# Kernel tuning notes

Measured on AMD Instinct MI355X. Metric: run time of the kernel, lower is better.

## Reference

```python
import jax, jax.numpy as jnp
import numpy as np

B, N, F, E = 2048, 64, 32, 5
U1, U2, UA = 128, 64, 128

def setup_inputs() -> dict:
    key = jax.random.key(0)
    ks = jax.random.split(key, 16)
    inp = {
        'adjacency': jax.random.uniform(ks[0], (B, N, N, E), dtype=jnp.float32),
        'hidden': jnp.zeros((B, 1), dtype=jnp.float32),
        'node': jax.random.normal(ks[1], (B, N, F), dtype=jnp.float32),
        # conv layer 1: per-edge-type dense F->U1 (stacked), plus node dense F->U1
        'W1': jax.random.normal(ks[2], (E - 1, F, U1), dtype=jnp.float32) * 0.05,
        'b1': jnp.zeros((E - 1, U1), dtype=jnp.float32),
        'V1': jax.random.normal(ks[3], (F, U1), dtype=jnp.float32) * 0.05,
        'c1': jnp.zeros((U1,), dtype=jnp.float32),
        # conv layer 2: annotations (U1+F)->U2, node F->U2
        'W2': jax.random.normal(ks[4], (E - 1, U1 + F, U2), dtype=jnp.float32) * 0.05,
        'b2': jnp.zeros((E - 1, U2), dtype=jnp.float32),
        'V2': jax.random.normal(ks[5], (F, U2), dtype=jnp.float32) * 0.05,
        'c2': jnp.zeros((U2,), dtype=jnp.float32),
        # aggregation: (U2+F)->UA gates
        'Wi': jax.random.normal(ks[6], (U2 + F, UA), dtype=jnp.float32) * 0.05,
        'bi': jnp.zeros((UA,), dtype=jnp.float32),
        'Wj': jax.random.normal(ks[7], (U2 + F, UA), dtype=jnp.float32) * 0.05,
        'bj': jnp.zeros((UA,), dtype=jnp.float32),
    }
    return inp


def _gconv(adj_t, annotations, node, W, b, V, c):
    # adj_t: [B,E-1,N,N]; annotations: [B,N,Fa]; node: [B,N,F]
    h = jnp.einsum('bnf,efu->benu', annotations, W) + b[None, :, None, :]
    h = jnp.einsum('bemn,benu->bemu', adj_t, h)          # adjacency-weighted sum
    out = h.sum(axis=1) + node @ V + c                   # [B,N,U]
    return jnp.tanh(out)


def reference(adjacency, hidden, node, W1, b1, V1, c1, W2, b2, V2, c2, Wi, bi, Wj, bj):
    # drop edge type 0, transpose to [B,E-1,N,N]
    adj_t = jnp.transpose(adjacency[:, :, :, 1:], (0, 3, 1, 2))
    # hidden is rank-2 at entry -> first layer uses node only
    h1 = _gconv(adj_t, node, node, W1, b1, V1, c1)                       # [B,N,U1]
    h2 = _gconv(adj_t, jnp.concatenate((h1, node), -1), node, W2, b2, V2, c2)  # [B,N,U2]
    # encoder-level annotations: (output, node) since hidden is rank-2
    ann = jnp.concatenate((h2, node), -1)                                # [B,N,U2+F]
    i = jax.nn.sigmoid(ann @ Wi + bi)
    j = jnp.tanh(ann @ Wj + bj)
    out = jnp.tanh(jnp.sum(i * j, axis=1))                               # [B,UA]
    return out
```

## Files before the change

kernel.cpp:

```cpp
#include <hip/hip_runtime.h>

typedef _Float16 f16;
typedef f16  f16x8 __attribute__((ext_vector_type(8)));
typedef f16  f16x4 __attribute__((ext_vector_type(4)));
typedef float f32x4 __attribute__((ext_vector_type(4)));
typedef unsigned int u32;

#define W1T_HI 0
#define W1T_LO 16384
#define V1T_HI 32768
#define V1T_LO 36864
#define W2T_HI 40960
#define W2T_LO 81920
#define V2T_HI 122880
#define V2T_LO 124928
#define WIT_HI 126976
#define WIT_LO 139264
#define WJT_HI 151552
#define WJT_LO 163840
#define WS_SRC 88064

#define ADJB_HI 0
#define ADJB_LO 32768
#define ANNB_HI 49152
#define ANNB_LO 65536
#define PTB     73728
#define LDS_BYTES 81920

__device__ __forceinline__ f32x4 mfma16(f16x8 a, f16x8 b, f32x4 c){
  return __builtin_amdgcn_mfma_f32_16x16x32_f16(a, b, c, 0, 0, 0);
}
__device__ __forceinline__ float fast_tanh(float x){
  float e = __expf(2.f * x);
  return 1.f - 2.f * __builtin_amdgcn_rcpf(e + 1.f);
}
__device__ __forceinline__ float fast_sigmoid(float x){
  return __builtin_amdgcn_rcpf(1.f + __expf(-x));
}

__device__ __forceinline__ unsigned char enc1(float lo){
  f16 h = (f16)lo;
  unsigned short u = __builtin_bit_cast(unsigned short, h);
  return (unsigned char)(((u32)u + 0x80u) >> 8);
}
__device__ __forceinline__ void enc8(unsigned char* p, const float* lo){
  u32 a = 0, b = 0;
  #pragma unroll
  for (int j = 0; j < 4; ++j) a |= (u32)enc1(lo[j]) << (8*j);
  #pragma unroll
  for (int j = 0; j < 4; ++j) b |= (u32)enc1(lo[4+j]) << (8*j);
  uint2 v = {a, b};
  *(uint2*)p = v;
}
__device__ __forceinline__ u32 enc4(const float* lo){
  return (u32)enc1(lo[0]) | ((u32)enc1(lo[1]) << 8)
       | ((u32)enc1(lo[2]) << 16) | ((u32)enc1(lo[3]) << 24);
}
__device__ __forceinline__ f16x8 dec8(const unsigned char* p){
  uint2 d = *(const uint2*)p;
  u32 w[4];
  w[0] = __builtin_amdgcn_perm(0u, d.x, 0x010c000cu);
  w[1] = __builtin_amdgcn_perm(0u, d.x, 0x030c020cu);
  w[2] = __builtin_amdgcn_perm(0u, d.y, 0x010c000cu);
  w[3] = __builtin_amdgcn_perm(0u, d.y, 0x030c020cu);
  f16x8 r; __builtin_memcpy(&r, w, 16);
  return r;
}

__global__ void prep_weights(const float* __restrict__ W1, const float* __restrict__ V1,
                             const float* __restrict__ W2, const float* __restrict__ V2,
                             const float* __restrict__ Wi, const float* __restrict__ Wj,
                             f16* __restrict__ ws){
  int i = blockIdx.x * 256 + threadIdx.x;
  if (i >= WS_SRC) return;
  float v; int hi_off, lo_off, idx;
  int j = i;
  if (j < 16384){ int e = j >> 12, u = (j >> 5) & 127, f = j & 31;
    v = W1[(e*32 + f)*128 + u]; hi_off = W1T_HI; lo_off = W1T_LO; idx = j; }
  else if ((j -= 16384) < 4096){ int u = j >> 5, f = j & 31;
    v = V1[f*128 + u]; hi_off = V1T_HI; lo_off = V1T_LO; idx = j; }
  else if ((j -= 4096) < 40960){ int e = j / 10240, r = j % 10240, u = r / 160, k = r % 160;
    v = W2[e*10240 + k*64 + u]; hi_off = W2T_HI; lo_off = W2T_LO; idx = j; }
  else if ((j -= 40960) < 2048){ int u = j >> 5, f = j & 31;
    v = V2[f*64 + u]; hi_off = V2T_HI; lo_off = V2T_LO; idx = j; }
  else if ((j -= 2048) < 12288){ int ua = j / 96, k = j % 96;
    v = Wi[k*128 + ua]; hi_off = WIT_HI; lo_off = WIT_LO; idx = j; }
  else { j -= 12288; int ua = j / 96, k = j % 96;
    v = Wj[k*128 + ua]; hi_off = WJT_HI; lo_off = WJT_LO; idx = j; }
  f16 h = (f16)v;
  ws[hi_off + idx] = h;
  ws[lo_off + idx] = (f16)(v - (float)h);
}

__global__ __launch_bounds__(512, 4) void encoder_main(
    const float* __restrict__ adj, const float* __restrict__ node,
    const float* __restrict__ b1, const float* __restrict__ c1,
    const float* __restrict__ b2, const float* __restrict__ c2,
    const float* __restrict__ bi, const float* __restrict__ bj,
    const f16* __restrict__ wb, float* __restrict__ out)
{
  extern __shared__ unsigned char ldsb[];
  f16* adjh            = (f16*)(ldsb + ADJB_HI);
  unsigned char* adjl  = ldsb + ADJB_LO;
  f16* annh            = (f16*)(ldsb + ANNB_HI);
  unsigned char* annl  = ldsb + ANNB_LO;
  float* scr           = (float*)(ldsb + ANNB_HI);
  f16* nodeH           = (f16*)(ldsb + PTB);
  f16* nodeLo          = (f16*)(ldsb + PTB + 4096);

  const int tid  = threadIdx.x;
  const int w    = tid >> 6;
  const int lane = tid & 63;
  const int q    = lane >> 4;
  const int l15  = lane & 15;
  const int eg   = w >> 2;
  const int w4   = w & 3;
  const int b    = blockIdx.x;
  const f32x4 z4 = {0.f, 0.f, 0.f, 0.f};

  unsigned char* ptb = ldsb + ((w < 4) ? (PTB + w*2048) : (ANNB_HI + (w - 4)*2048));
  unsigned char* ptl = ldsb + ANNB_LO + w*1024;
  const int ptrow  = l15 * 128;
  const int ptlrow = l15 * 64;

  {
    const float* ap = adj + (size_t)b * 20480;
    #pragma unroll
    for (int i = 0; i < 4; ++i){
      int fu = tid + 512*i;
      int e = fu >> 9, m = (fu >> 3) & 63, uc = fu & 7;
      const float* p = ap + (m*64 + uc*8)*5 + e + 1;
      float v[8], lo[8]; f16x8 hi;
      #pragma unroll
      for (int jj = 0; jj < 8; ++jj) v[jj] = p[jj*5];
      #pragma unroll
      for (int jj = 0; jj < 8; ++jj){
        f16 h = (f16)v[jj]; hi[jj] = h; lo[jj] = v[jj] - (float)h;
      }
      int off = e*4096 + m*64 + ((uc ^ (m & 7)) * 8);
      *(f16x8*)&adjh[off] = hi;
      enc8(&adjl[off], lo);
    }
    if (tid < 256){
      const float* np = node + (size_t)b * 2048 + (tid & 63)*32 + (tid >> 6)*8;
      float4 a = *(const float4*)np, c = *(const float4*)(np + 4);
      float v[8] = {a.x, a.y, a.z, a.w, c.x, c.y, c.z, c.w};
      f16x8 hi, lo;
      #pragma unroll
      for (int jj = 0; jj < 8; ++jj){
        f16 h = (f16)v[jj]; hi[jj] = h; lo[jj] = (f16)(v[jj] - (float)h);
      }
      int n = tid & 63, un = tid >> 6;
      *(f16x8*)&nodeH [n*32 + ((un ^ (n & 3)) * 8)] = hi;
      *(f16x8*)&nodeLo[n*32 + ((un ^ (n & 3)) * 8)] = lo;
    }
  }
  __syncthreads();

  f16x8 anh[4], anl[4];
  #pragma unroll
  for (int mt = 0; mt < 4; ++mt){
    anh[mt] = *(const f16x8*)&nodeH [(mt*16 + l15)*32 + ((q ^ (l15 & 3)) * 8)];
    anl[mt] = *(const f16x8*)&nodeLo[(mt*16 + l15)*32 + ((q ^ (l15 & 3)) * 8)];
  }
  __syncthreads();

  f32x4 acc1[4][2];
  #pragma unroll
  for (int mt = 0; mt < 4; ++mt){ acc1[mt][0] = z4; acc1[mt][1] = z4; }

  #pragma unroll
  for (int i = 0; i < 2; ++i){
    const int e = eg*2 + i;
    #pragma unroll
    for (int ut = 0; ut < 2; ++ut){
      const int u = w4*32 + ut*16 + l15;
      f16x8 wh = *(const f16x8*)&wb[W1T_HI + (e*128 + u)*32 + q*8];
      f16x8 wl = *(const f16x8*)&wb[W1T_LO + (e*128 + u)*32 + q*8];
      float bias = b1[e*128 + u];
      #pragma unroll
      for (int mt = 0; mt < 4; ++mt){
        f32x4 pf = mfma16(anh[mt], wh, z4);
        pf = mfma16(anl[mt], wh, pf);
        pf = mfma16(anh[mt], wl, pf);
        f16x4 ph; float lo4[4];
        #pragma unroll
        for (int r = 0; r < 4; ++r){
          float v = pf[r] + bias;
          f16 h = (f16)v; ph[r] = h; lo4[r] = v - (float)h;
        }
        int unit = ((mt*2 + (q >> 1)) ^ (l15 & 7));
        *(f16x4*)(ptb + ptrow + unit*16 + (q & 1)*8) = ph;
        *(u32*)(ptl + ptlrow + unit*8 + (q & 1)*4) = enc4(lo4);
      }
      #pragma unroll
      for (int ks = 0; ks < 2; ++ks){
        int pu = ((ks*4 + q) ^ (l15 & 7));
        f16x8 bph = *(const f16x8*)(ptb + ptrow + pu*16);
        f16x8 bpl = dec8(ptl + ptlrow + pu*8);
        #pragma unroll
        for (int mt = 0; mt < 4; ++mt){
          int off = e*4096 + (mt*16 + l15)*64 + (((ks*4 + q) ^ (l15 & 7)) * 8);
          f16x8 ah = *(const f16x8*)&adjh[off];
          f16x8 al = dec8(&adjl[off]);
          acc1[mt][ut] = mfma16(ah, bph, acc1[mt][ut]);
          acc1[mt][ut] = mfma16(al, bph, acc1[mt][ut]);
          acc1[mt][ut] = mfma16(ah, bpl, acc1[mt][ut]);
        }
      }
    }
  }
  __syncthreads();

  if (eg == 0){
    #pragma unroll
    for (int ut = 0; ut < 2; ++ut){
      const int u = w4*32 + ut*16 + l15;
      f16x8 wh = *(const f16x8*)&wb[V1T_HI + u*32 + q*8];
      f16x8 wl = *(const f16x8*)&wb[V1T_LO + u*32 + q*8];
      #pragma unroll
      for (int mt = 0; mt < 4; ++mt){
        acc1[mt][ut] = mfma16(anh[mt], wh, acc1[mt][ut]);
        acc1[mt][ut] = mfma16(anl[mt], wh, acc1[mt][ut]);
        acc1[mt][ut] = mfma16(anh[mt], wl, acc1[mt][ut]);
      }
    }
  } else {
    #pragma unroll
    for (int mt = 0; mt < 4; ++mt)
      #pragma unroll
      for (int ut = 0; ut < 2; ++ut)
        #pragma unroll
        for (int r = 0; r < 4; ++r){
          int n = mt*16 + q*4 + r;
          int u = w4*32 + ut*16 + l15;
          scr[n*128 + (u ^ ((n & 4) << 2))] = acc1[mt][ut][r];
        }
  }
  __syncthreads();
  if (eg == 0){
    #pragma unroll
    for (int mt = 0; mt < 4; ++mt)
      #pragma unroll
      for (int ut = 0; ut < 2; ++ut)
        #pragma unroll
        for (int r = 0; r < 4; ++r){
          int n = mt*16 + q*4 + r;
          int u = w4*32 + ut*16 + l15;
          acc1[mt][ut][r] += scr[n*128 + (u ^ ((n & 4) << 2))];
        }
  }
  __syncthreads();
  if (eg == 0){
    #pragma unroll
    for (int ut = 0; ut < 2; ++ut){
      const int u = w4*32 + ut*16 + l15;
      float cv = c1[u];
      #pragma unroll
      for (int mt = 0; mt < 4; ++mt)
        #pragma unroll
        for (int r = 0; r < 4; ++r){
          float h = fast_tanh(acc1[mt][ut][r] + cv);
          f16 hh = (f16)h;
          int row = mt*16 + q*4 + r;
          int unit = ((u >> 3) ^ (row & 7));
          annh[row*128 + unit*8 + (u & 7)] = hh;
          annl[row*128 + unit*8 + (u & 7)] = enc1(h - (float)hh);
        }
    }
  }
  __syncthreads();

  const int u2 = w4*16 + l15;
  f32x4 qf[2][4];
  #pragma unroll
  for (int mt = 0; mt < 4; ++mt){
    #pragma unroll
    for (int i = 0; i < 2; ++i){
      const int e = eg*2 + i;
      const f16* w2h = &wb[W2T_HI + (e*64 + u2)*160];
      const f16* w2l = &wb[W2T_LO + (e*64 + u2)*160];
      f16x8 wnh = *(const f16x8*)&w2h[4*32 + q*8];
      f16x8 wnl = *(const f16x8*)&w2l[4*32 + q*8];
      f32x4 t = mfma16(anh[mt], wnh, z4);
      t = mfma16(anl[mt], wnh, t);
      t = mfma16(anh[mt], wnl, t);
      #pragma unroll
      for (int ks = 0; ks < 4; ++ks){
        int off = (mt*16 + l15)*128 + (((ks*4 + q) ^ (l15 & 7)) * 8);
        f16x8 axh = *(const f16x8*)&annh[off];
        f16x8 axl = dec8(&annl[off]);
        f16x8 wh = *(const f16x8*)&w2h[ks*32 + q*8];
        f16x8 wl = *(const f16x8*)&w2l[ks*32 + q*8];
        t = mfma16(axh, wh, t);
        t = mfma16(axl, wh, t);
        t = mfma16(axh, wl, t);
      }
      qf[i][mt] = t;
    }
  }
  __syncthreads();

  f32x4 acc2[4];
  #pragma unroll
  for (int mt = 0; mt < 4; ++mt) acc2[mt] = z4;
  #pragma unroll
  for (int i = 0; i < 2; ++i){
    const int e = eg*2 + i;
    float bias = b2[e*64 + u2];
    #pragma unroll
    for (int mt = 0; mt < 4; ++mt){
      f16x4 ph; float lo4[4];
      #pragma unroll
      for (int r = 0; r < 4; ++r){
        float v = qf[i][mt][r] + bias;
        f16 h = (f16)v; ph[r] = h; lo4[r] = v - (float)h;
      }
      int unit = ((mt*2 + (q >> 1)) ^ (l15 & 7));
      *(f16x4*)(ptb + ptrow + unit*16 + (q & 1)*8) = ph;
      *(u32*)(ptl + ptlrow + unit*8 + (q & 1)*4) = enc4(lo4);
    }
    #pragma unroll
    for (int ks = 0; ks < 2; ++ks){
      int pu = ((ks*4 + q) ^ (l15 & 7));
      f16x8 bph = *(const f16x8*)(ptb + ptrow + pu*16);
      f16x8 bpl = dec8(ptl + ptlrow + pu*8);
      #pragma unroll
      for (int mt = 0; mt < 4; ++mt){
        int off = e*4096 + (mt*16 + l15)*64 + (((ks*4 + q) ^ (l15 & 7)) * 8);
        f16x8 ah = *(const f16x8*)&adjh[off];
        f16x8 al = dec8(&adjl[off]);
        acc2[mt] = mfma16(ah, bph, acc2[mt]);
        acc2[mt] = mfma16(al, bph, acc2[mt]);
        acc2[mt] = mfma16(ah, bpl, acc2[mt]);
      }
    }
  }
  __syncthreads();
  if (eg == 0){
    f16x8 wh = *(const f16x8*)&wb[V2T_HI + u2*32 + q*8];
    f16x8 wl = *(const f16x8*)&wb[V2T_LO + u2*32 + q*8];
    #pragma unroll
    for (int mt = 0; mt < 4; ++mt){
      acc2[mt] = mfma16(anh[mt], wh, acc2[mt]);
      acc2[mt] = mfma16(anl[mt], wh, acc2[mt]);
      acc2[mt] = mfma16(anh[mt], wl, acc2[mt]);
    }
  } else {
    #pragma unroll
    for (int mt = 0; mt < 4; ++mt)
      #pragma unroll
      for (int r = 0; r < 4; ++r){
        int n = mt*16 + q*4 + r;
        scr[n*64 + (u2 ^ ((n & 4) << 2))] = acc2[mt][r];
      }
  }
  __syncthreads();
  if (eg == 0){
    #pragma unroll
    for (int mt = 0; mt < 4; ++mt)
      #pragma unroll
      for (int r = 0; r < 4; ++r){
        int n = mt*16 + q*4 + r;
        acc2[mt][r] += scr[n*64 + (u2 ^ ((n & 4) << 2))];
      }
  }
  __syncthreads();
  if (eg == 0){
    float cv = c2[u2];
    const int uc = 64 + u2;
    #pragma unroll
    for (int mt = 0; mt < 4; ++mt)
      #pragma unroll
      for (int r = 0; r < 4; ++r){
        float h = fast_tanh(acc2[mt][r] + cv);
        f16 hh = (f16)h;
        int row = mt*16 + q*4 + r;
        int unit = ((uc >> 3) ^ (row & 7));
        annh[row*128 + unit*8 + (uc & 7)] = hh;
        annl[row*128 + unit*8 + (uc & 7)] = enc1(h - (float)hh);
      }
  }
  __syncthreads();

  const int ua = w*16 + l15;
  float bib = bi[ua], bjb = bj[ua];
  f32x4 iacc[4], jacc[4];
  #pragma unroll
  for (int mt = 0; mt < 4; ++mt){ iacc[mt] = z4; jacc[mt] = z4; }
  #pragma unroll
  for (int ks = 0; ks < 3; ++ks){
    f16x8 wih = *(const f16x8*)&wb[WIT_HI + ua*96 + ks*32 + q*8];
    f16x8 wil = *(const f16x8*)&wb[WIT_LO + ua*96 + ks*32 + q*8];
    f16x8 wjh = *(const f16x8*)&wb[WJT_HI + ua*96 + ks*32 + q*8];
    f16x8 wjl = *(const f16x8*)&wb[WJT_LO + ua*96 + ks*32 + q*8];
    if (ks < 2){
      #pragma unroll
      for (int mt = 0; mt < 4; ++mt){
        int off = (mt*16 + l15)*128 + (((8 + ks*4 + q) ^ (l15 & 7)) * 8);
        f16x8 gh = *(const f16x8*)&annh[off];
        f16x8 gl = dec8(&annl[off]);
        iacc[mt] = mfma16(gh, wih, iacc[mt]);
        iacc[mt] = mfma16(gl, wih, iacc[mt]);
        iacc[mt] = mfma16(gh, wil, iacc[mt]);
        jacc[mt] = mfma16(gh, wjh, jacc[mt]);
        jacc[mt] = mfma16(gl, wjh, jacc[mt]);
        jacc[mt] = mfma16(gh, wjl, jacc[mt]);
      }
    } else {
      #pragma unroll
      for (int mt = 0; mt < 4; ++mt){
        iacc[mt] = mfma16(anh[mt], wih, iacc[mt]);
        iacc[mt] = mfma16(anl[mt], wih, iacc[mt]);
        iacc[mt] = mfma16(anh[mt], wil, iacc[mt]);
        jacc[mt] = mfma16(anh[mt], wjh, jacc[mt]);
        jacc[mt] = mfma16(anl[mt], wjh, jacc[mt]);
        jacc[mt] = mfma16(anh[mt], wjl, jacc[mt]);
      }
    }
  }
  float s = 0.f;
  #pragma unroll
  for (int mt = 0; mt < 4; ++mt)
    #pragma unroll
    for (int r = 0; r < 4; ++r)
      s += fast_sigmoid(iacc[mt][r] + bib) * fast_tanh(jacc[mt][r] + bjb);
  s += __shfl_xor(s, 16);
  s += __shfl_xor(s, 32);
  if (q == 0) out[(size_t)b*128 + ua] = fast_tanh(s);
}

extern "C" void kernel_launch(void* const* d_in, const int* in_sizes, int n_in,
                              void* d_out, int out_size, void* d_ws, size_t ws_size,
                              hipStream_t stream) {
  (void)in_sizes; (void)n_in; (void)out_size; (void)ws_size;
  const float* adj  = (const float*)d_in[0];
  const float* node = (const float*)d_in[2];
  const float* W1   = (const float*)d_in[3];
  const float* b1   = (const float*)d_in[4];
  const float* V1   = (const float*)d_in[5];
  const float* c1   = (const float*)d_in[6];
  const float* W2   = (const float*)d_in[7];
  const float* b2   = (const float*)d_in[8];
  const float* V2   = (const float*)d_in[9];
  const float* c2   = (const float*)d_in[10];
  const float* Wi   = (const float*)d_in[11];
  const float* bi   = (const float*)d_in[12];
  const float* Wj   = (const float*)d_in[13];
  const float* bj   = (const float*)d_in[14];
  f16* wb    = (f16*)d_ws;
  float* out = (float*)d_out;

  hipFuncSetAttribute((const void*)encoder_main,
                      hipFuncAttributeMaxDynamicSharedMemorySize, LDS_BYTES);

  prep_weights<<<(WS_SRC + 255) / 256, 256, 0, stream>>>(W1, V1, W2, V2, Wi, Wj, wb);
  encoder_main<<<2048, 512, LDS_BYTES, stream>>>(adj, node, b1, c1, b2, c2, bi, bj, wb, out);
}
```

Before: 388.4 us.

## Reload node tiles from LDS on demand and shrink layer-1 reduction scratch

Removes the long-lived register copies of the node fragments (anh/anl). The node hi/lo tiles are kept in LDS and reloaded with volatile loads at each use, and the adjacency fragments are also read with volatile loads to stop the compiler hoisting them. All per-wave P-tile scratch now lives in the ANN region, and the cross-eg layer-1 reduction is split into two half-width passes so the scratch is 64 columns wide. The layer-2 node/annotation GEMM loop is reordered so both edge types share each weight load. The goal is lower VGPR pressure, which may allow higher occupancy, at the cost of extra LDS traffic and two more barriers.

```diff
diff --git a/kernel.cpp b/kernel.cpp
--- a/kernel.cpp
+++ b/kernel.cpp
@@ -5,6 +5,7 @@
 typedef f16  f16x4 __attribute__((ext_vector_type(4)));
 typedef float f32x4 __attribute__((ext_vector_type(4)));
 typedef unsigned int u32;
+typedef unsigned long long u64;
 
 #define W1T_HI 0
 #define W1T_LO 16384
@@ -56,13 +57,27 @@
   return (u32)enc1(lo[0]) | ((u32)enc1(lo[1]) << 8)
        | ((u32)enc1(lo[2]) << 16) | ((u32)enc1(lo[3]) << 24);
 }
+__device__ __forceinline__ f16x8 dec8_w(u32 dx, u32 dy){
+  u32 w[4];
+  w[0] = __builtin_amdgcn_perm(0u, dx, 0x010c000cu);
+  w[1] = __builtin_amdgcn_perm(0u, dx, 0x030c020cu);
+  w[2] = __builtin_amdgcn_perm(0u, dy, 0x010c000cu);
+  w[3] = __builtin_amdgcn_perm(0u, dy, 0x030c020cu);
+  f16x8 r; __builtin_memcpy(&r, w, 16);
+  return r;
+}
 __device__ __forceinline__ f16x8 dec8(const unsigned char* p){
   uint2 d = *(const uint2*)p;
-  u32 w[4];
-  w[0] = __builtin_amdgcn_perm(0u, d.x, 0x010c000cu);
-  w[1] = __builtin_amdgcn_perm(0u, d.x, 0x030c020cu);
-  w[2] = __builtin_amdgcn_perm(0u, d.y, 0x010c000cu);
-  w[3] = __builtin_amdgcn_perm(0u, d.y, 0x030c020cu);
+  return dec8_w(d.x, d.y);
+}
+__device__ __forceinline__ f16x8 dec8v(const unsigned char* p){
+  u64 v = *(const volatile u64*)p;
+  return dec8_w((u32)v, (u32)(v >> 32));
+}
+__device__ __forceinline__ f16x8 lds16v(const f16* p){
+  u64 a = ((const volatile u64*)p)[0];
+  u64 b = ((const volatile u64*)p)[1];
+  u64 w[2] = {a, b};
   f16x8 r; __builtin_memcpy(&r, w, 16);
   return r;
 }
@@ -118,10 +133,15 @@
   const int b    = blockIdx.x;
   const f32x4 z4 = {0.f, 0.f, 0.f, 0.f};
 
-  unsigned char* ptb = ldsb + ((w < 4) ? (PTB + w*2048) : (ANNB_HI + (w - 4)*2048));
+  unsigned char* ptb = ldsb + ANNB_HI + w*2048;
   unsigned char* ptl = ldsb + ANNB_LO + w*1024;
   const int ptrow  = l15 * 128;
   const int ptlrow = l15 * 64;
+
+  #define LOAD_NODE(mt, nh, nl) {                                   \
+    int no_ = ((mt)*16 + l15)*32 + ((q ^ (l15 & 3)) * 8);           \
+    nh = lds16v(&nodeH[no_]);                                       \
+    nl = lds16v(&nodeLo[no_]); }
 
   {
     const float* ap = adj + (size_t)b * 20480;
@@ -157,14 +177,6 @@
   }
   __syncthreads();
 
-  f16x8 anh[4], anl[4];
-  #pragma unroll
-  for (int mt = 0; mt < 4; ++mt){
-    anh[mt] = *(const f16x8*)&nodeH [(mt*16 + l15)*32 + ((q ^ (l15 & 3)) * 8)];
-    anl[mt] = *(const f16x8*)&nodeLo[(mt*16 + l15)*32 + ((q ^ (l15 & 3)) * 8)];
-  }
-  __syncthreads();
-
   f32x4 acc1[4][2];
   #pragma unroll
   for (int mt = 0; mt < 4; ++mt){ acc1[mt][0] = z4; acc1[mt][1] = z4; }
@@ -180,9 +192,10 @@
       float bias = b1[e*128 + u];
       #pragma unroll
       for (int mt = 0; mt < 4; ++mt){
-        f32x4 pf = mfma16(anh[mt], wh, z4);
-        pf = mfma16(anl[mt], wh, pf);
-        pf = mfma16(anh[mt], wl, pf);
+        f16x8 nh, nl; LOAD_NODE(mt, nh, nl);
+        f32x4 pf = mfma16(nh, wh, z4);
+        pf = mfma16(nl, wh, pf);
+        pf = mfma16(nh, wl, pf);
         f16x4 ph; float lo4[4];
         #pragma unroll
         for (int r = 0; r < 4; ++r){
@@ -201,8 +214,8 @@
         #pragma unroll
         for (int mt = 0; mt < 4; ++mt){
           int off = e*4096 + (mt*16 + l15)*64 + (((ks*4 + q) ^ (l15 & 7)) * 8);
-          f16x8 ah = *(const f16x8*)&adjh[off];
-          f16x8 al = dec8(&adjl[off]);
+          f16x8 ah = lds16v(&adjh[off]);
+          f16x8 al = dec8v(&adjl[off]);
           acc1[mt][ut] = mfma16(ah, bph, acc1[mt][ut]);
           acc1[mt][ut] = mfma16(al, bph, acc1[mt][ut]);
           acc1[mt][ut] = mfma16(ah, bpl, acc1[mt][ut]);
@@ -220,12 +233,13 @@
       f16x8 wl = *(const f16x8*)&wb[V1T_LO + u*32 + q*8];
       #pragma unroll
       for (int mt = 0; mt < 4; ++mt){
-        acc1[mt][ut] = mfma16(anh[mt], wh, acc1[mt][ut]);
-        acc1[mt][ut] = mfma16(anl[mt], wh, acc1[mt][ut]);
-        acc1[mt][ut] = mfma16(anh[mt], wl, acc1[mt][ut]);
-      }
-    }
-  } else {
+        f16x8 nh, nl; LOAD_NODE(mt, nh, nl);
+        acc1[mt][ut] = mfma16(nh, wh, acc1[mt][ut]);
+        acc1[mt][ut] = mfma16(nl, wh, acc1[mt][ut]);
+        acc1[mt][ut] = mfma16(nh, wl, acc1[mt][ut]);
+      }
+    }
+  } else if (w4 < 2){
     #pragma unroll
     for (int mt = 0; mt < 4; ++mt)
       #pragma unroll
@@ -233,12 +247,12 @@
         #pragma unroll
         for (int r = 0; r < 4; ++r){
           int n = mt*16 + q*4 + r;
-          int u = w4*32 + ut*16 + l15;
-          scr[n*128 + (u ^ ((n & 4) << 2))] = acc1[mt][ut][r];
-        }
-  }
-  __syncthreads();
-  if (eg == 0){
+          int ul = w4*32 + ut*16 + l15;
+          scr[n*64 + (ul ^ ((n & 4) << 2))] = acc1[mt][ut][r];
+        }
+  }
+  __syncthreads();
+  if (eg == 0 && w4 < 2){
     #pragma unroll
     for (int mt = 0; mt < 4; ++mt)
       #pragma unroll
@@ -246,8 +260,34 @@
         #pragma unroll
         for (int r = 0; r < 4; ++r){
           int n = mt*16 + q*4 + r;
-          int u = w4*32 + ut*16 + l15;
-          acc1[mt][ut][r] += scr[n*128 + (u ^ ((n & 4) << 2))];
+          int ul = w4*32 + ut*16 + l15;
+          acc1[mt][ut][r] += scr[n*64 + (ul ^ ((n & 4) << 2))];
+        }
+  }
+  __syncthreads();
+  if (eg == 1 && w4 >= 2){
+    #pragma unroll
+    for (int mt = 0; mt < 4; ++mt)
+      #pragma unroll
+      for (int ut = 0; ut < 2; ++ut)
+        #pragma unroll
+        for (int r = 0; r < 4; ++r){
+          int n = mt*16 + q*4 + r;
+          int ul = (w4 - 2)*32 + ut*16 + l15;
+          scr[n*64 + (ul ^ ((n & 4) << 2))] = acc1[mt][ut][r];
+        }
+  }
+  __syncthreads();
+  if (eg == 0 && w4 >= 2){
+    #pragma unroll
+    for (int mt = 0; mt < 4; ++mt)
+      #pragma unroll
+      for (int ut = 0; ut < 2; ++ut)
+        #pragma unroll
+        for (int r = 0; r < 4; ++r){
+          int n = mt*16 + q*4 + r;
+          int ul = (w4 - 2)*32 + ut*16 + l15;
+          acc1[mt][ut][r] += scr[n*64 + (ul ^ ((n & 4) << 2))];
         }
   }
   __syncthreads();
@@ -272,31 +312,46 @@
   __syncthreads();
 
   const int u2 = w4*16 + l15;
+  const int e0 = eg*2, e1 = eg*2 + 1;
+  const f16* w2h0 = &wb[W2T_HI + (e0*64 + u2)*160];
+  const f16* w2l0 = &wb[W2T_LO + (e0*64 + u2)*160];
+  const f16* w2h1 = &wb[W2T_HI + (e1*64 + u2)*160];
+  const f16* w2l1 = &wb[W2T_LO + (e1*64 + u2)*160];
   f32x4 qf[2][4];
-  #pragma unroll
-  for (int mt = 0; mt < 4; ++mt){
-    #pragma unroll
-    for (int i = 0; i < 2; ++i){
-      const int e = eg*2 + i;
-      const f16* w2h = &wb[W2T_HI + (e*64 + u2)*160];
-      const f16* w2l = &wb[W2T_LO + (e*64 + u2)*160];
-      f16x8 wnh = *(const f16x8*)&w2h[4*32 + q*8];
-      f16x8 wnl = *(const f16x8*)&w2l[4*32 + q*8];
-      f32x4 t = mfma16(anh[mt], wnh, z4);
-      t = mfma16(anl[mt], wnh, t);
-      t = mfma16(anh[mt], wnl, t);
-      #pragma unroll
-      for (int ks = 0; ks < 4; ++ks){
-        int off = (mt*16 + l15)*128 + (((ks*4 + q) ^ (l15 & 7)) * 8);
-        f16x8 axh = *(const f16x8*)&annh[off];
-        f16x8 axl = dec8(&annl[off]);
-        f16x8 wh = *(const f16x8*)&w2h[ks*32 + q*8];
-        f16x8 wl = *(const f16x8*)&w2l[ks*32 + q*8];
-        t = mfma16(axh, wh, t);
-        t = mfma16(axl, wh, t);
-        t = mfma16(axh, wl, t);
-      }
-      qf[i][mt] = t;
+  {
+    f16x8 wA = *(const f16x8*)&w2h0[128 + q*8];
+    f16x8 wB = *(const f16x8*)&w2l0[128 + q*8];
+    f16x8 wC = *(const f16x8*)&w2h1[128 + q*8];
+    f16x8 wD = *(const f16x8*)&w2l1[128 + q*8];
+    #pragma unroll
+    for (int mt = 0; mt < 4; ++mt){
+      f16x8 nh, nl; LOAD_NODE(mt, nh, nl);
+      f32x4 t0 = mfma16(nh, wA, z4);
+      t0 = mfma16(nl, wA, t0);
+      t0 = mfma16(nh, wB, t0);
+      f32x4 t1 = mfma16(nh, wC, z4);
+      t1 = mfma16(nl, wC, t1);
+      t1 = mfma16(nh, wD, t1);
+      qf[0][mt] = t0; qf[1][mt] = t1;
+    }
+  }
+  #pragma unroll
+  for (int ks = 0; ks < 4; ++ks){
+    f16x8 wA = *(const f16x8*)&w2h0[ks*32 + q*8];
+    f16x8 wB = *(const f16x8*)&w2l0[ks*32 + q*8];
+    f16x8 wC = *(const f16x8*)&w2h1[ks*32 + q*8];
+    f16x8 wD = *(const f16x8*)&w2l1[ks*32 + q*8];
+    #pragma unroll
+    for (int mt = 0; mt < 4; ++mt){
+      int off = (mt*16 + l15)*128 + (((ks*4 + q) ^ (l15 & 7)) * 8);
+      f16x8 axh = *(const f16x8*)&annh[off];
+      f16x8 axl = dec8(&annl[off]);
+      qf[0][mt] = mfma16(axh, wA, qf[0][mt]);
+      qf[0][mt] = mfma16(axl, wA, qf[0][mt]);
+      qf[0][mt] = mfma16(axh, wB, qf[0][mt]);
+      qf[1][mt] = mfma16(axh, wC, qf[1][mt]);
+      qf[1][mt] = mfma16(axl, wC, qf[1][mt]);
+      qf[1][mt] = mfma16(axh, wD, qf[1][mt]);
     }
   }
   __syncthreads();
@@ -342,9 +397,10 @@
     f16x8 wl = *(const f16x8*)&wb[V2T_LO + u2*32 + q*8];
     #pragma unroll
     for (int mt = 0; mt < 4; ++mt){
-      acc2[mt] = mfma16(anh[mt], wh, acc2[mt]);
-      acc2[mt] = mfma16(anl[mt], wh, acc2[mt]);
-      acc2[mt] = mfma16(anh[mt], wl, acc2[mt]);
+      f16x8 nh, nl; LOAD_NODE(mt, nh, nl);
+      acc2[mt] = mfma16(nh, wh, acc2[mt]);
+      acc2[mt] = mfma16(nl, wh, acc2[mt]);
+      acc2[mt] = mfma16(nh, wl, acc2[mt]);
     }
   } else {
     #pragma unroll
@@ -410,12 +466,13 @@
     } else {
       #pragma unroll
       for (int mt = 0; mt < 4; ++mt){
-        iacc[mt] = mfma16(anh[mt], wih, iacc[mt]);
-        iacc[mt] = mfma16(anl[mt], wih, iacc[mt]);
-        iacc[mt] = mfma16(anh[mt], wil, iacc[mt]);
-        jacc[mt] = mfma16(anh[mt], wjh, jacc[mt]);
-        jacc[mt] = mfma16(anl[mt], wjh, jacc[mt]);
-        jacc[mt] = mfma16(anh[mt], wjl, jacc[mt]);
+        f16x8 nh, nl; LOAD_NODE(mt, nh, nl);
+        iacc[mt] = mfma16(nh, wih, iacc[mt]);
+        iacc[mt] = mfma16(nl, wih, iacc[mt]);
+        iacc[mt] = mfma16(nh, wil, iacc[mt]);
+        jacc[mt] = mfma16(nh, wjh, jacc[mt]);
+        jacc[mt] = mfma16(nl, wjh, jacc[mt]);
+        jacc[mt] = mfma16(nh, wjl, jacc[mt]);
       }
     }
   }
@@ -428,6 +485,7 @@
   s += __shfl_xor(s, 16);
   s += __shfl_xor(s, 32);
   if (q == 0) out[(size_t)b*128 + ua] = fast_tanh(s);
+  #undef LOAD_NODE
 }
 
 extern "C" void kernel_launch(void* const* d_in, const int* in_sizes, int n_in,
```

New measurement: 550.9 us. +41.8%, slower.

## Double block to 1024 threads and repartition work across 16 waves

Applied to the files above, without the earlier changes.

Raises the workgroup from 8 to 16 waves and gives each wave a smaller slice of every stage: one U1 tile per wave in layer 1, one edge type per wave group in layer 2, and half the node rows in aggregation. LDS grows to 128KB with dedicated per-wave scratch and separate partial-sum buffers, which removes some reduction barriers. The aim is more parallelism and shorter serial MFMA chains per wave. The cost is roughly one resident block per CU, which limits overlap of the adjacency load with compute, plus an extra cross-wave reduction at the end.

```diff
diff --git a/kernel.cpp b/kernel.cpp
--- a/kernel.cpp
+++ b/kernel.cpp
@@ -24,8 +24,10 @@
 #define ADJB_LO 32768
 #define ANNB_HI 49152
 #define ANNB_LO 65536
-#define PTB     73728
-#define LDS_BYTES 81920
+#define NODEB   73728
+#define PTHB    81920
+#define PTLB    114688
+#define LDS_BYTES 131072
 
 __device__ __forceinline__ f32x4 mfma16(f16x8 a, f16x8 b, f32x4 c){
   return __builtin_amdgcn_mfma_f32_16x16x32_f16(a, b, c, 0, 0, 0);
@@ -92,7 +94,7 @@
   ws[lo_off + idx] = (f16)(v - (float)h);
 }
 
-__global__ __launch_bounds__(512, 4) void encoder_main(
+__global__ __launch_bounds__(1024, 4) void encoder_main(
     const float* __restrict__ adj, const float* __restrict__ node,
     const float* __restrict__ b1, const float* __restrict__ c1,
     const float* __restrict__ b2, const float* __restrict__ c2,
@@ -104,30 +106,29 @@
   unsigned char* adjl  = ldsb + ADJB_LO;
   f16* annh            = (f16*)(ldsb + ANNB_HI);
   unsigned char* annl  = ldsb + ANNB_LO;
-  float* scr           = (float*)(ldsb + ANNB_HI);
-  f16* nodeH           = (f16*)(ldsb + PTB);
-  f16* nodeLo          = (f16*)(ldsb + PTB + 4096);
+  f16* nodeH           = (f16*)(ldsb + NODEB);
+  f16* nodeLo          = (f16*)(ldsb + NODEB + 4096);
+  float* scr           = (float*)(ldsb + PTHB);
 
   const int tid  = threadIdx.x;
   const int w    = tid >> 6;
   const int lane = tid & 63;
   const int q    = lane >> 4;
   const int l15  = lane & 15;
-  const int eg   = w >> 2;
-  const int w4   = w & 3;
+  const int eg   = w >> 3;
   const int b    = blockIdx.x;
   const f32x4 z4 = {0.f, 0.f, 0.f, 0.f};
 
-  unsigned char* ptb = ldsb + ((w < 4) ? (PTB + w*2048) : (ANNB_HI + (w - 4)*2048));
-  unsigned char* ptl = ldsb + ANNB_LO + w*1024;
+  unsigned char* ptb = ldsb + PTHB + w*2048;
+  unsigned char* ptl = ldsb + PTLB + w*1024;
   const int ptrow  = l15 * 128;
   const int ptlrow = l15 * 64;
 
   {
     const float* ap = adj + (size_t)b * 20480;
     #pragma unroll
-    for (int i = 0; i < 4; ++i){
-      int fu = tid + 512*i;
+    for (int i = 0; i < 2; ++i){
+      int fu = tid + 1024*i;
       int e = fu >> 9, m = (fu >> 3) & 63, uc = fu & 7;
       const float* p = ap + (m*64 + uc*8)*5 + e + 1;
       float v[8], lo[8]; f16x8 hi;
@@ -163,157 +164,27 @@
     anh[mt] = *(const f16x8*)&nodeH [(mt*16 + l15)*32 + ((q ^ (l15 & 3)) * 8)];
     anl[mt] = *(const f16x8*)&nodeLo[(mt*16 + l15)*32 + ((q ^ (l15 & 3)) * 8)];
   }
-  __syncthreads();
-
-  f32x4 acc1[4][2];
-  #pragma unroll
-  for (int mt = 0; mt < 4; ++mt){ acc1[mt][0] = z4; acc1[mt][1] = z4; }
+
+  const int u1 = (w & 7)*16 + l15;
+  f32x4 acc1[4];
+  #pragma unroll
+  for (int mt = 0; mt < 4; ++mt) acc1[mt] = z4;
 
   #pragma unroll
   for (int i = 0; i < 2; ++i){
     const int e = eg*2 + i;
-    #pragma unroll
-    for (int ut = 0; ut < 2; ++ut){
-      const int u = w4*32 + ut*16 + l15;
-      f16x8 wh = *(const f16x8*)&wb[W1T_HI + (e*128 + u)*32 + q*8];
-      f16x8 wl = *(const f16x8*)&wb[W1T_LO + (e*128 + u)*32 + q*8];
-      float bias = b1[e*128 + u];
-      #pragma unroll
-      for (int mt = 0; mt < 4; ++mt){
-        f32x4 pf = mfma16(anh[mt], wh, z4);
-        pf = mfma16(anl[mt], wh, pf);
-        pf = mfma16(anh[mt], wl, pf);
-        f16x4 ph; float lo4[4];
-        #pragma unroll
-        for (int r = 0; r < 4; ++r){
-          float v = pf[r] + bias;
-          f16 h = (f16)v; ph[r] = h; lo4[r] = v - (float)h;
-        }
-        int unit = ((mt*2 + (q >> 1)) ^ (l15 & 7));
-        *(f16x4*)(ptb + ptrow + unit*16 + (q & 1)*8) = ph;
-        *(u32*)(ptl + ptlrow + unit*8 + (q & 1)*4) = enc4(lo4);
-      }
-      #pragma unroll
-      for (int ks = 0; ks < 2; ++ks){
-        int pu = ((ks*4 + q) ^ (l15 & 7));
-        f16x8 bph = *(const f16x8*)(ptb + ptrow + pu*16);
-        f16x8 bpl = dec8(ptl + ptlrow + pu*8);
-        #pragma unroll
-        for (int mt = 0; mt < 4; ++mt){
-          int off = e*4096 + (mt*16 + l15)*64 + (((ks*4 + q) ^ (l15 & 7)) * 8);
-          f16x8 ah = *(const f16x8*)&adjh[off];
-          f16x8 al = dec8(&adjl[off]);
-          acc1[mt][ut] = mfma16(ah, bph, acc1[mt][ut]);
-          acc1[mt][ut] = mfma16(al, bph, acc1[mt][ut]);
-          acc1[mt][ut] = mfma16(ah, bpl, acc1[mt][ut]);
-        }
-      }
-    }
-  }
-  __syncthreads();
-
-  if (eg == 0){
-    #pragma unroll
-    for (int ut = 0; ut < 2; ++ut){
-      const int u = w4*32 + ut*16 + l15;
-      f16x8 wh = *(const f16x8*)&wb[V1T_HI + u*32 + q*8];
-      f16x8 wl = *(const f16x8*)&wb[V1T_LO + u*32 + q*8];
-      #pragma unroll
-      for (int mt = 0; mt < 4; ++mt){
-        acc1[mt][ut] = mfma16(anh[mt], wh, acc1[mt][ut]);
-        acc1[mt][ut] = mfma16(anl[mt], wh, acc1[mt][ut]);
-        acc1[mt][ut] = mfma16(anh[mt], wl, acc1[mt][ut]);
-      }
-    }
-  } else {
-    #pragma unroll
-    for (int mt = 0; mt < 4; ++mt)
-      #pragma unroll
-      for (int ut = 0; ut < 2; ++ut)
-        #pragma unroll
-        for (int r = 0; r < 4; ++r){
-          int n = mt*16 + q*4 + r;
-          int u = w4*32 + ut*16 + l15;
-          scr[n*128 + (u ^ ((n & 4) << 2))] = acc1[mt][ut][r];
-        }
-  }
-  __syncthreads();
-  if (eg == 0){
-    #pragma unroll
-    for (int mt = 0; mt < 4; ++mt)
-      #pragma unroll
-      for (int ut = 0; ut < 2; ++ut)
-        #pragma unroll
-        for (int r = 0; r < 4; ++r){
-          int n = mt*16 + q*4 + r;
-          int u = w4*32 + ut*16 + l15;
-          acc1[mt][ut][r] += scr[n*128 + (u ^ ((n & 4) << 2))];
-        }
-  }
-  __syncthreads();
-  if (eg == 0){
-    #pragma unroll
-    for (int ut = 0; ut < 2; ++ut){
-      const int u = w4*32 + ut*16 + l15;
-      float cv = c1[u];
-      #pragma unroll
-      for (int mt = 0; mt < 4; ++mt)
-        #pragma unroll
-        for (int r = 0; r < 4; ++r){
-          float h = fast_tanh(acc1[mt][ut][r] + cv);
-          f16 hh = (f16)h;
-          int row = mt*16 + q*4 + r;
-          int unit = ((u >> 3) ^ (row & 7));
-          annh[row*128 + unit*8 + (u & 7)] = hh;
-          annl[row*128 + unit*8 + (u & 7)] = enc1(h - (float)hh);
-        }
-    }
-  }
-  __syncthreads();
-
-  const int u2 = w4*16 + l15;
-  f32x4 qf[2][4];
-  #pragma unroll
-  for (int mt = 0; mt < 4; ++mt){
-    #pragma unroll
-    for (int i = 0; i < 2; ++i){
-      const int e = eg*2 + i;
-      const f16* w2h = &wb[W2T_HI + (e*64 + u2)*160];
-      const f16* w2l = &wb[W2T_LO + (e*64 + u2)*160];
-      f16x8 wnh = *(const f16x8*)&w2h[4*32 + q*8];
-      f16x8 wnl = *(const f16x8*)&w2l[4*32 + q*8];
-      f32x4 t = mfma16(anh[mt], wnh, z4);
-      t = mfma16(anl[mt], wnh, t);
-      t = mfma16(anh[mt], wnl, t);
-      #pragma unroll
-      for (int ks = 0; ks < 4; ++ks){
-        int off = (mt*16 + l15)*128 + (((ks*4 + q) ^ (l15 & 7)) * 8);
-        f16x8 axh = *(const f16x8*)&annh[off];
-        f16x8 axl = dec8(&annl[off]);
-        f16x8 wh = *(const f16x8*)&w2h[ks*32 + q*8];
-        f16x8 wl = *(const f16x8*)&w2l[ks*32 + q*8];
-        t = mfma16(axh, wh, t);
-        t = mfma16(axl, wh, t);
-        t = mfma16(axh, wl, t);
-      }
-      qf[i][mt] = t;
-    }
-  }
-  __syncthreads();
-
-  f32x4 acc2[4];
-  #pragma unroll
-  for (int mt = 0; mt < 4; ++mt) acc2[mt] = z4;
-  #pragma unroll
-  for (int i = 0; i < 2; ++i){
-    const int e = eg*2 + i;
-    float bias = b2[e*64 + u2];
-    #pragma unroll
-    for (int mt = 0; mt < 4; ++mt){
+    f16x8 wh = *(const f16x8*)&wb[W1T_HI + (e*128 + u1)*32 + q*8];
+    f16x8 wl = *(const f16x8*)&wb[W1T_LO + (e*128 + u1)*32 + q*8];
+    float bias = b1[e*128 + u1];
+    #pragma unroll
+    for (int mt = 0; mt < 4; ++mt){
+      f32x4 pf = mfma16(anh[mt], wh, z4);
+      pf = mfma16(anl[mt], wh, pf);
+      pf = mfma16(anh[mt], wl, pf);
       f16x4 ph; float lo4[4];
       #pragma unroll
       for (int r = 0; r < 4; ++r){
-        float v = qf[i][mt][r] + bias;
+        float v = pf[r] + bias;
         f16 h = (f16)v; ph[r] = h; lo4[r] = v - (float)h;
       }
       int unit = ((mt*2 + (q >> 1)) ^ (l15 & 7));
@@ -328,6 +199,106 @@
       #pragma unroll
       for (int mt = 0; mt < 4; ++mt){
         int off = e*4096 + (mt*16 + l15)*64 + (((ks*4 + q) ^ (l15 & 7)) * 8);
+        f16x8 ah = *(const f16x8*)&adjh[off];
+        f16x8 al = dec8(&adjl[off]);
+        acc1[mt] = mfma16(ah, bph, acc1[mt]);
+        acc1[mt] = mfma16(al, bph, acc1[mt]);
+        acc1[mt] = mfma16(ah, bpl, acc1[mt]);
+      }
+    }
+  }
+  __syncthreads();
+
+  if (eg == 1){
+    #pragma unroll
+    for (int mt = 0; mt < 4; ++mt)
+      #pragma unroll
+      for (int r = 0; r < 4; ++r){
+        int n = mt*16 + q*4 + r;
+        scr[n*128 + (u1 ^ ((n & 4) << 2))] = acc1[mt][r];
+      }
+  } else {
+    f16x8 wh = *(const f16x8*)&wb[V1T_HI + u1*32 + q*8];
+    f16x8 wl = *(const f16x8*)&wb[V1T_LO + u1*32 + q*8];
+    #pragma unroll
+    for (int mt = 0; mt < 4; ++mt){
+      acc1[mt] = mfma16(anh[mt], wh, acc1[mt]);
+      acc1[mt] = mfma16(anl[mt], wh, acc1[mt]);
+      acc1[mt] = mfma16(anh[mt], wl, acc1[mt]);
+    }
+  }
+  __syncthreads();
+  if (eg == 0){
+    float cv = c1[u1];
+    #pragma unroll
+    for (int mt = 0; mt < 4; ++mt)
+      #pragma unroll
+      for (int r = 0; r < 4; ++r){
+        int n = mt*16 + q*4 + r;
+        float h = fast_tanh(acc1[mt][r] + scr[n*128 + (u1 ^ ((n & 4) << 2))] + cv);
+        f16 hh = (f16)h;
+        int unit = ((u1 >> 3) ^ (n & 7));
+        annh[n*128 + unit*8 + (u1 & 7)] = hh;
+        annl[n*128 + unit*8 + (u1 & 7)] = enc1(h - (float)hh);
+      }
+  }
+  __syncthreads();
+
+  const int e2 = eg*2 + ((w >> 2) & 1);
+  const int u2 = (w & 3)*16 + l15;
+  const f16* w2h = &wb[W2T_HI + (e2*64 + u2)*160];
+  const f16* w2l = &wb[W2T_LO + (e2*64 + u2)*160];
+  f32x4 qf[4];
+  {
+    f16x8 wnh = *(const f16x8*)&w2h[128 + q*8];
+    f16x8 wnl = *(const f16x8*)&w2l[128 + q*8];
+    #pragma unroll
+    for (int mt = 0; mt < 4; ++mt){
+      f32x4 t = mfma16(anh[mt], wnh, z4);
+      t = mfma16(anl[mt], wnh, t);
+      t = mfma16(anh[mt], wnl, t);
+      qf[mt] = t;
+    }
+  }
+  #pragma unroll
+  for (int ks = 0; ks < 4; ++ks){
+    f16x8 wh = *(const f16x8*)&w2h[ks*32 + q*8];
+    f16x8 wl = *(const f16x8*)&w2l[ks*32 + q*8];
+    #pragma unroll
+    for (int mt = 0; mt < 4; ++mt){
+      int off = (mt*16 + l15)*128 + (((ks*4 + q) ^ (l15 & 7)) * 8);
+      f16x8 axh = *(const f16x8*)&annh[off];
+      f16x8 axl = dec8(&annl[off]);
+      qf[mt] = mfma16(axh, wh, qf[mt]);
+      qf[mt] = mfma16(axl, wh, qf[mt]);
+      qf[mt] = mfma16(axh, wl, qf[mt]);
+    }
+  }
+  f32x4 acc2[4];
+  #pragma unroll
+  for (int mt = 0; mt < 4; ++mt) acc2[mt] = z4;
+  {
+    float bias = b2[e2*64 + u2];
+    #pragma unroll
+    for (int mt = 0; mt < 4; ++mt){
+      f16x4 ph; float lo4[4];
+      #pragma unroll
+      for (int r = 0; r < 4; ++r){
+        float v = qf[mt][r] + bias;
+        f16 h = (f16)v; ph[r] = h; lo4[r] = v - (float)h;
+      }
+      int unit = ((mt*2 + (q >> 1)) ^ (l15 & 7));
+      *(f16x4*)(ptb + ptrow + unit*16 + (q & 1)*8) = ph;
+      *(u32*)(ptl + ptlrow + unit*8 + (q & 1)*4) = enc4(lo4);
+    }
+    #pragma unroll
+    for (int ks = 0; ks < 2; ++ks){
+      int pu = ((ks*4 + q) ^ (l15 & 7));
+      f16x8 bph = *(const f16x8*)(ptb + ptrow + pu*16);
+      f16x8 bpl = dec8(ptl + ptlrow + pu*8);
+      #pragma unroll
+      for (int mt = 0; mt < 4; ++mt){
+        int off = e2*4096 + (mt*16 + l15)*64 + (((ks*4 + q) ^ (l15 & 7)) * 8);
         f16x8 ah = *(const f16x8*)&adjh[off];
         f16x8 al = dec8(&adjl[off]);
         acc2[mt] = mfma16(ah, bph, acc2[mt]);
@@ -337,7 +308,8 @@
     }
   }
   __syncthreads();
-  if (eg == 0){
+
+  if (e2 == 0){
     f16x8 wh = *(const f16x8*)&wb[V2T_HI + u2*32 + q*8];
     f16x8 wl = *(const f16x8*)&wb[V2T_LO + u2*32 + q*8];
     #pragma unroll
@@ -347,47 +319,46 @@
       acc2[mt] = mfma16(anh[mt], wl, acc2[mt]);
     }
   } else {
+    float* s2 = (e2 == 1) ? (float*)(ldsb + PTHB)
+              : (e2 == 2) ? (float*)(ldsb + PTHB + 16384)
+                          : (float*)(ldsb + PTLB);
     #pragma unroll
     for (int mt = 0; mt < 4; ++mt)
       #pragma unroll
       for (int r = 0; r < 4; ++r){
         int n = mt*16 + q*4 + r;
-        scr[n*64 + (u2 ^ ((n & 4) << 2))] = acc2[mt][r];
-      }
-  }
-  __syncthreads();
-  if (eg == 0){
-    #pragma unroll
-    for (int mt = 0; mt < 4; ++mt)
-      #pragma unroll
-      for (int r = 0; r < 4; ++r){
-        int n = mt*16 + q*4 + r;
-        acc2[mt][r] += scr[n*64 + (u2 ^ ((n & 4) << 2))];
-      }
-  }
-  __syncthreads();
-  if (eg == 0){
+        s2[n*64 + (u2 ^ ((n & 4) << 2))] = acc2[mt][r];
+      }
+  }
+  __syncthreads();
+  if (e2 == 0){
+    const float* p0 = (const float*)(ldsb + PTHB);
+    const float* p1 = (const float*)(ldsb + PTHB + 16384);
+    const float* p2 = (const float*)(ldsb + PTLB);
     float cv = c2[u2];
     const int uc = 64 + u2;
     #pragma unroll
     for (int mt = 0; mt < 4; ++mt)
       #pragma unroll
       for (int r = 0; r < 4; ++r){
-        float h = fast_tanh(acc2[mt][r] + cv);
+        int n = mt*16 + q*4 + r;
+        int so = n*64 + (u2 ^ ((n & 4) << 2));
+        float h = fast_tanh(acc2[mt][r] + p0[so] + p1[so] + p2[so] + cv);
         f16 hh = (f16)h;
-        int row = mt*16 + q*4 + r;
-        int unit = ((uc >> 3) ^ (row & 7));
-        annh[row*128 + unit*8 + (uc & 7)] = hh;
-        annl[row*128 + unit*8 + (uc & 7)] = enc1(h - (float)hh);
-      }
-  }
-  __syncthreads();
-
-  const int ua = w*16 + l15;
+        int unit = ((uc >> 3) ^ (n & 7));
+        annh[n*128 + unit*8 + (uc & 7)] = hh;
+        annl[n*128 + unit*8 + (uc & 7)] = enc1(h - (float)hh);
+      }
+  }
+  __syncthreads();
+
+  const int ua  = (w & 7)*16 + l15;
+  const int mth = w >> 3;
+  f16x8 n0h = mth ? anh[2] : anh[0], n0l = mth ? anl[2] : anl[0];
+  f16x8 n1h = mth ? anh[3] : anh[1], n1l = mth ? anl[3] : anl[1];
   float bib = bi[ua], bjb = bj[ua];
-  f32x4 iacc[4], jacc[4];
-  #pragma unroll
-  for (int mt = 0; mt < 4; ++mt){ iacc[mt] = z4; jacc[mt] = z4; }
+  f32x4 iacc[2], jacc[2];
+  iacc[0] = z4; iacc[1] = z4; jacc[0] = z4; jacc[1] = z4;
   #pragma unroll
   for (int ks = 0; ks < 3; ++ks){
     f16x8 wih = *(const f16x8*)&wb[WIT_HI + ua*96 + ks*32 + q*8];
@@ -396,38 +367,46 @@
     f16x8 wjl = *(const f16x8*)&wb[WJT_LO + ua*96 + ks*32 + q*8];
     if (ks < 2){
       #pragma unroll
-      for (int mt = 0; mt < 4; ++mt){
+      for (int j = 0; j < 2; ++j){
+        int mt = mth*2 + j;
         int off = (mt*16 + l15)*128 + (((8 + ks*4 + q) ^ (l15 & 7)) * 8);
         f16x8 gh = *(const f16x8*)&annh[off];
         f16x8 gl = dec8(&annl[off]);
-        iacc[mt] = mfma16(gh, wih, iacc[mt]);
-        iacc[mt] = mfma16(gl, wih, iacc[mt]);
-        iacc[mt] = mfma16(gh, wil, iacc[mt]);
-        jacc[mt] = mfma16(gh, wjh, jacc[mt]);
-        jacc[mt] = mfma16(gl, wjh, jacc[mt]);
-        jacc[mt] = mfma16(gh, wjl, jacc[mt]);
+        iacc[j] = mfma16(gh, wih, iacc[j]);
+        iacc[j] = mfma16(gl, wih, iacc[j]);
+        iacc[j] = mfma16(gh, wil, iacc[j]);
+        jacc[j] = mfma16(gh, wjh, jacc[j]);
+        jacc[j] = mfma16(gl, wjh, jacc[j]);
+        jacc[j] = mfma16(gh, wjl, jacc[j]);
       }
     } else {
-      #pragma unroll
-      for (int mt = 0; mt < 4; ++mt){
-        iacc[mt] = mfma16(anh[mt], wih, iacc[mt]);
-        iacc[mt] = mfma16(anl[mt], wih, iacc[mt]);
-        iacc[mt] = mfma16(anh[mt], wil, iacc[mt]);
-        jacc[mt] = mfma16(anh[mt], wjh, jacc[mt]);
-        jacc[mt] = mfma16(anl[mt], wjh, jacc[mt]);
-        jacc[mt] = mfma16(anh[mt], wjl, jacc[mt]);
-      }
+      iacc[0] = mfma16(n0h, wih, iacc[0]);
+      iacc[0] = mfma16(n0l, wih, iacc[0]);
+      iacc[0] = mfma16(n0h, wil, iacc[0]);
+      jacc[0] = mfma16(n0h, wjh, jacc[0]);
+      jacc[0] = mfma16(n0l, wjh, jacc[0]);
+      jacc[0] = mfma16(n0h, wjl, jacc[0]);
+      iacc[1] = mfma16(n1h, wih, iacc[1]);
+      iacc[1] = mfma16(n1l, wih, iacc[1]);
+      iacc[1] = mfma16(n1h, wil, iacc[1]);
+      jacc[1] = mfma16(n1h, wjh, jacc[1]);
+      jacc[1] = mfma16(n1l, wjh, jacc[1]);
+      jacc[1] = mfma16(n1h, wjl, jacc[1]);
     }
   }
   float s = 0.f;
   #pragma unroll
-  for (int mt = 0; mt < 4; ++mt)
+  for (int j = 0; j < 2; ++j)
     #pragma unroll
     for (int r = 0; r < 4; ++r)
-      s += fast_sigmoid(iacc[mt][r] + bib) * fast_tanh(jacc[mt][r] + bjb);
+      s += fast_sigmoid(iacc[j][r] + bib) * fast_tanh(jacc[j][r] + bjb);
   s += __shfl_xor(s, 16);
   s += __shfl_xor(s, 32);
-  if (q == 0) out[(size_t)b*128 + ua] = fast_tanh(s);
+  float* pex = (float*)(ldsb + PTHB);
+  if (q == 0) pex[mth*128 + ua] = s;
+  __syncthreads();
+  if (mth == 0 && q == 0)
+    out[(size_t)b*128 + ua] = fast_tanh(s + pex[128 + ua]);
 }
 
 extern "C" void kernel_launch(void* const* d_in, const int* in_sizes, int n_in,
@@ -455,5 +434,5 @@
                       hipFuncAttributeMaxDynamicSharedMemorySize, LDS_BYTES);
 
   prep_weights<<<(WS_SRC + 255) / 256, 256, 0, stream>>>(W1, V1, W2, V2, Wi, Wj, wb);
-  encoder_main<<<2048, 512, LDS_BYTES, stream>>>(adj, node, b1, c1, b2, c2, bi, bj, wb, out);
-}
+  encoder_main<<<2048, 1024, LDS_BYTES, stream>>>(adj, node, b1, c1, b2, c2, bi, bj, wb, out);
+}
```

Result: slower. 433.4 us (+11.6%).
